# Optimization experiments

Measured on AMD Instinct MI355X. Metric: run time of the kernel, lower is better.

## Reference

```python
import jax, jax.numpy as jnp
import numpy as np

N, B, T, D, H = 200, 100, 256, 5, 20  # count_lstms, batch, seq_len, io units, lstm units


def setup_inputs() -> dict:
    key = jax.random.key(0)
    ks = jax.random.split(key, 4)
    inputs = jax.random.normal(ks[0], (B, T, D), dtype=jnp.float32)
    # Stacked per-LSTM parameters (Keras gate order: i, f, c, o)
    W = jax.random.normal(ks[1], (N, D, 4 * H), dtype=jnp.float32) * (1.0 / np.sqrt(D))
    U = jax.random.normal(ks[2], (N, H, 4 * H), dtype=jnp.float32) * (1.0 / np.sqrt(H))
    b = jnp.zeros((N, 4 * H), dtype=jnp.float32)
    dense_W = jax.random.normal(ks[3], (N * H, D), dtype=jnp.float32) * (1.0 / np.sqrt(N * H))
    dense_b = jnp.zeros((D,), dtype=jnp.float32)
    return {"inputs": inputs, "W": W, "U": U, "b": b, "dense_W": dense_W, "dense_b": dense_b}


def reference(inputs, W, U, b, dense_W, dense_b):
    # inputs: [B, T, D]; W: [N, D, 4H]; U: [N, H, 4H]; b: [N, 4H]
    n, h = W.shape[0], U.shape[1]
    batch = inputs.shape[0]
    x_t = jnp.transpose(inputs, (1, 0, 2))  # [T, B, D]
    h0 = jnp.zeros((n, batch, h), dtype=inputs.dtype)
    c0 = jnp.zeros((n, batch, h), dtype=inputs.dtype)

    def step(carry, xt):
        hprev, cprev = carry
        # gates for all N lstms at once: [N, B, 4H]
        z = (jnp.einsum('bd,ndk->nbk', xt, W)
             + jnp.einsum('nbh,nhk->nbk', hprev, U)
             + b[:, None, :])
        zi, zf, zg, zo = jnp.split(z, 4, axis=-1)
        i = jax.nn.sigmoid(zi)
        f = jax.nn.sigmoid(zf)
        g = jnp.tanh(zg)
        o = jax.nn.sigmoid(zo)
        cnew = f * cprev + i * g
        hnew = o * jnp.tanh(cnew)
        return (hnew, cnew), hnew

    (_, _), hs = jax.lax.scan(step, (h0, c0), x_t)  # hs: [T, N, B, H]
    # concat along feature axis -> [B, T, N*H]
    concat = jnp.transpose(hs, (2, 0, 1, 3)).reshape(batch, x_t.shape[0], n * h)
    out = concat @ dense_W + dense_b  # [B, T, D]
    return out
```

## Files before the change

kernel.cpp:

```cpp
#include <hip/hip_runtime.h>
#include <math.h>

constexpr int NL = 200;
constexpr int B  = 100;
constexpr int T  = 256;
constexpr int D  = 5;
constexpr int H  = 20;
constexpr int NW = 7;
constexpr int KP = 40;
constexpr int NWAVE = 5;
constexpr int BLKT  = 64 * NWAVE;
constexpr int BPAD  = 112;

constexpr int KX = 24;

typedef float  f32x4  __attribute__((ext_vector_type(4)));
typedef short  bf16x8 __attribute__((ext_vector_type(8)));

__device__ __forceinline__ float rcpf(float x) { return __builtin_amdgcn_rcpf(x); }

#if __has_builtin(__builtin_amdgcn_exp2f)
__device__ __forceinline__ float exp2fast(float x) { return __builtin_amdgcn_exp2f(x); }
#else
__device__ __forceinline__ float exp2fast(float x) { return __expf(x * 0.6931471805599453f); }
#endif

__device__ __forceinline__ unsigned short f2bf(float f) {
    union { float f; unsigned u; } v; v.f = f;
    unsigned r = v.u + 0x7fffu + ((v.u >> 16) & 1u);
    return (unsigned short)(r >> 16);
}
__device__ __forceinline__ unsigned pk2bf(float lo, float hi) {
    return (unsigned)f2bf(lo) | ((unsigned)f2bf(hi) << 16);
}

__device__ __forceinline__ void block_sync_lds() {
    asm volatile("s_waitcnt lgkmcnt(0)" ::: "memory");
    __builtin_amdgcn_s_barrier();
}

constexpr float NLOG2E = -1.4426950408889634f;
constexpr float TLOG2E = 2.8853900817779268f;

__global__ __launch_bounds__(256) void init_out_kernel(const float* __restrict__ dense_b,
                                                       float* __restrict__ out, int n) {
    int i = blockIdx.x * 256 + threadIdx.x;
    if (i < n) out[i] = dense_b[i % D];
}

__global__ __launch_bounds__(256) void xpack_kernel(const float* __restrict__ x,
                                                    int4* __restrict__ xe) {
    int i = blockIdx.x * 256 + threadIdx.x;
    if (i >= T * BPAD) return;
    const int t = i / BPAD;
    const int b = i % BPAD;
    int4 v = {0, 0, 0, 0};
    if (b < B) {
        const float* s = x + ((size_t)b * T + t) * D;
        v.x = (int)pk2bf(s[0], s[1]);
        v.y = (int)pk2bf(s[2], s[3]);
        v.z = (int)pk2bf(s[4], 0.0f);
        v.w = 0x00003F80;
    }
    xe[i] = v;
}

template<bool USE_WS>
__global__ __attribute__((amdgpu_flat_work_group_size(BLKT, BLKT)))
void lstm_mfma5_kernel(
    const int4*  __restrict__ xe,
    const float* __restrict__ Wg,
    const float* __restrict__ Ug,
    const float* __restrict__ bg,
    const float* __restrict__ dWg,
    float* __restrict__ pw,
    float* __restrict__ out)
{
    const int blk = blockIdx.x;
    const int n   = blk / NW;
    const int w   = blk % NW;
    const int tid = threadIdx.x;
    const int wid = tid >> 6;
    const int l   = tid & 63;
    const int c16 = l & 15;
    const int g4  = l >> 4;

    __shared__ __align__(16) short bcol[2][16][KP];

    for (int i = tid; i < 2 * 16 * KP / 2; i += BLKT)
        ((int*)&bcol[0][0][0])[i] = 0;

    const float* Un = Ug  + (size_t)n * H * 4 * H;
    const float* Wn = Wg  + (size_t)n * D * 4 * H;
    const float* bn = bg  + (size_t)n * 4 * H;
    const float* dn = dWg + (size_t)n * H * D;

    const int gateA = c16 & 3;
    const int hA4   = c16 >> 2;
    const float sA  = (gateA == 2) ? TLOG2E : NLOG2E;
    const int colA  = gateA * H + (wid * 4 + hA4);
    bf16x8 afrag;
    #pragma unroll
    for (int j = 0; j < 8; ++j) {
        const int k = 8 * g4 + j;
        float v = 0.0f;
        if (k < KX) {
            const int mt = k % 6, gg = k / 6;
            if (mt < 5) v = Un[(mt * 4 + gg) * 4 * H + colA];
        } else if (k < KX + D) {
            v = Wn[(k - KX) * 4 * H + colA];
        } else if (k == 30) {
            v = bn[colA];
        }
        afrag[j] = (short)f2bf(sA * v);
    }
    bf16x8 afrag_d = {};
    if (wid == 1) {
        #pragma unroll
        for (int j = 0; j < 8; ++j) {
            const int k = 8 * g4 + j;
            float v = 0.0f;
            if (c16 < D && k < KX) {
                const int mt = k % 6, gg = k / 6;
                if (mt < 5) v = dn[(mt * 4 + gg) * D + c16];
            }
            afrag_d[j] = (short)f2bf(v);
        }
    }

    const int  bgl    = w * 16 + c16;
    const bool bvalid = bgl < B;
    const int4* xq = xe + bgl;
    float* pwn = USE_WS ? (pw + (size_t)n * T * (D * B))
                        : (out + ((size_t)bgl * T) * D);

    __syncthreads();

    int4 xn4;
    if (wid == 0 && l < 16) {
        *(int4*)&bcol[0][c16][KX] = xq[0];
        xn4 = xq[(T > 1 ? 1 : 0) * BPAD];
    }
    __syncthreads();

    float cst = 0.0f;
    const f32x4 zero4 = {0.0f, 0.0f, 0.0f, 0.0f};
    int p = 0;

    for (int t = 0; t < T; ++t) {
        const bf16x8 bfrag = *(const bf16x8*)&bcol[p][c16][8 * g4];

        if (wid == 1) {
            const f32x4 accd = __builtin_amdgcn_mfma_f32_16x16x32_bf16(
                afrag_d, bfrag, zero4, 0, 0, 0);
            if (t > 0 && bvalid) {
                #pragma unroll
                for (int reg = 0; reg < 4; ++reg) {
                    const int d = g4 * 4 + reg;
                    if (d < D) {
                        if (USE_WS)
                            pwn[(size_t)(t - 1) * (D * B) + d * B + bgl] = accd[reg];
                        else
                            atomicAdd(&pwn[(size_t)(t - 1) * D + d], accd[reg]);
                    }
                }
            }
        }

        const f32x4 acc = __builtin_amdgcn_mfma_f32_16x16x32_bf16(
            afrag, bfrag, zero4, 0, 0, 0);
        const float iv = rcpf(1.0f + exp2fast(acc[0]));
        const float fv = rcpf(1.0f + exp2fast(acc[1]));
        const float gv = fmaf(-2.0f, rcpf(exp2fast(acc[2]) + 1.0f), 1.0f);
        const float ov = rcpf(1.0f + exp2fast(acc[3]));
        cst = fmaf(fv, cst, iv * gv);
        const float th = fmaf(-2.0f, rcpf(exp2fast(TLOG2E * cst) + 1.0f), 1.0f);
        const float hv = ov * th;

        bcol[p ^ 1][c16][g4 * 6 + wid] = (short)f2bf(hv);

        if (wid == 0 && l < 16) {
            *(int4*)&bcol[p ^ 1][c16][KX] = xn4;
            const int tc = (t + 2 < T) ? t + 2 : T - 1;
            xn4 = xq[(size_t)tc * BPAD];
        }

        block_sync_lds();
        p ^= 1;
    }

    if (wid == 1) {
        const bf16x8 bfrag = *(const bf16x8*)&bcol[p][c16][8 * g4];
        const f32x4 accd = __builtin_amdgcn_mfma_f32_16x16x32_bf16(
            afrag_d, bfrag, zero4, 0, 0, 0);
        if (bvalid) {
            #pragma unroll
            for (int reg = 0; reg < 4; ++reg) {
                const int d = g4 * 4 + reg;
                if (d < D) {
                    if (USE_WS)
                        pwn[(size_t)(T - 1) * (D * B) + d * B + bgl] = accd[reg];
                    else
                        atomicAdd(&pwn[(size_t)(T - 1) * D + d], accd[reg]);
                }
            }
        }
    }
}

__global__ __launch_bounds__(512) void reduce_kernel(
    const float* __restrict__ pw, const float* __restrict__ dense_b,
    float* __restrict__ out)
{
    const int t    = blockIdx.x;
    const int flat = threadIdx.x;
    if (flat >= B * D) return;
    const int d = flat / B;
    const int b = flat % B;
    const float* p = pw + (size_t)t * (D * B) + flat;
    constexpr size_t stride = (size_t)T * D * B;
    float a0 = 0.0f, a1 = 0.0f;
    #pragma unroll 10
    for (int n = 0; n < NL; n += 2) {
        a0 += p[(size_t)n * stride];
        a1 += p[(size_t)(n + 1) * stride];
    }
    out[((size_t)b * T + t) * D + d] = a0 + a1 + dense_b[d];
}

extern "C" void kernel_launch(void* const* d_in, const int* in_sizes, int n_in,
                              void* d_out, int out_size, void* d_ws, size_t ws_size,
                              hipStream_t stream) {
    const float* x   = (const float*)d_in[0];
    const float* Wg  = (const float*)d_in[1];
    const float* Ug  = (const float*)d_in[2];
    const float* bg  = (const float*)d_in[3];
    const float* dWg = (const float*)d_in[4];
    const float* dbv = (const float*)d_in[5];
    float* out = (float*)d_out;

    const size_t xe_bytes = (size_t)T * BPAD * sizeof(int4);
    const size_t pw_bytes = (size_t)NL * T * D * B * sizeof(float);

    int4* xe = (int4*)d_ws;
    xpack_kernel<<<(T * BPAD + 255) / 256, 256, 0, stream>>>(x, xe);

    if (ws_size >= xe_bytes + pw_bytes) {
        float* pw = (float*)((char*)d_ws + xe_bytes);
        lstm_mfma5_kernel<true><<<NL * NW, BLKT, 0, stream>>>(xe, Wg, Ug, bg, dWg, pw, out);
        reduce_kernel<<<T, 512, 0, stream>>>(pw, dbv, out);
    } else {
        init_out_kernel<<<(out_size + 255) / 256, 256, 0, stream>>>(dbv, out, out_size);
        lstm_mfma5_kernel<false><<<NL * NW, BLKT, 0, stream>>>(xe, Wg, Ug, bg, dWg, nullptr, out);
    }
}
```

Baseline: 219.9 us.

## Process two LSTMs per block to interleave independent recurrences

Each block now runs two independent LSTMs (n and n+100) side by side, with separate LDS buffers and state, and issues two MFMAs plus two activation chains per timestep under one barrier. The goal is to hide the latency of the serial MFMA→transcendental→LDS→barrier chain with independent work and to halve the number of barriers overall. The cost is more registers and LDS per block and half as many blocks (700 instead of 1400), which may reduce parallelism across the GPU.

```diff
diff --git a/kernel.cpp b/kernel.cpp
--- a/kernel.cpp
+++ b/kernel.cpp
@@ -11,6 +11,7 @@
 constexpr int NWAVE = 5;
 constexpr int BLKT  = 64 * NWAVE;
 constexpr int BPAD  = 112;
+constexpr int NPAIR = NL / 2;
 
 constexpr int KX = 24;
 
@@ -65,9 +66,19 @@
     xe[i] = v;
 }
 
+__device__ __forceinline__ float lstm_act(const f32x4 a, float& c) {
+    const float iv = rcpf(1.0f + exp2fast(a[0]));
+    const float fv = rcpf(1.0f + exp2fast(a[1]));
+    const float gv = fmaf(-2.0f, rcpf(exp2fast(a[2]) + 1.0f), 1.0f);
+    const float ov = rcpf(1.0f + exp2fast(a[3]));
+    c = fmaf(fv, c, iv * gv);
+    const float th = fmaf(-2.0f, rcpf(exp2fast(TLOG2E * c) + 1.0f), 1.0f);
+    return ov * th;
+}
+
 template<bool USE_WS>
 __global__ __attribute__((amdgpu_flat_work_group_size(BLKT, BLKT)))
-void lstm_mfma5_kernel(
+void lstm_mfma5x2_kernel(
     const int4*  __restrict__ xe,
     const float* __restrict__ Wg,
     const float* __restrict__ Ug,
@@ -77,45 +88,49 @@
     float* __restrict__ out)
 {
     const int blk = blockIdx.x;
-    const int n   = blk / NW;
+    const int pr  = blk / NW;
     const int w   = blk % NW;
+    const int n0  = pr;
+    const int n1  = pr + NPAIR;
     const int tid = threadIdx.x;
     const int wid = tid >> 6;
     const int l   = tid & 63;
     const int c16 = l & 15;
     const int g4  = l >> 4;
 
-    __shared__ __align__(16) short bcol[2][16][KP];
-
-    for (int i = tid; i < 2 * 16 * KP / 2; i += BLKT)
-        ((int*)&bcol[0][0][0])[i] = 0;
-
-    const float* Un = Ug  + (size_t)n * H * 4 * H;
-    const float* Wn = Wg  + (size_t)n * D * 4 * H;
-    const float* bn = bg  + (size_t)n * 4 * H;
-    const float* dn = dWg + (size_t)n * H * D;
+    __shared__ __align__(16) short bcol[2][2][16][KP];
+
+    for (int i = tid; i < 2 * 2 * 16 * KP / 2; i += BLKT)
+        ((int*)&bcol[0][0][0][0])[i] = 0;
 
     const int gateA = c16 & 3;
     const int hA4   = c16 >> 2;
     const float sA  = (gateA == 2) ? TLOG2E : NLOG2E;
-    const int colA  = gateA * H + (wid * 4 + hA4);
-    bf16x8 afrag;
-    #pragma unroll
-    for (int j = 0; j < 8; ++j) {
-        const int k = 8 * g4 + j;
-        float v = 0.0f;
-        if (k < KX) {
-            const int mt = k % 6, gg = k / 6;
-            if (mt < 5) v = Un[(mt * 4 + gg) * 4 * H + colA];
-        } else if (k < KX + D) {
-            v = Wn[(k - KX) * 4 * H + colA];
-        } else if (k == 30) {
-            v = bn[colA];
-        }
-        afrag[j] = (short)f2bf(sA * v);
-    }
-    bf16x8 afrag_d = {};
-    if (wid == 1) {
+    auto buildA = [&](int n) {
+        const float* Un = Ug + (size_t)n * H * 4 * H;
+        const float* Wn = Wg + (size_t)n * D * 4 * H;
+        const float* bn = bg + (size_t)n * 4 * H;
+        const int colA  = gateA * H + (wid * 4 + hA4);
+        bf16x8 a;
+        #pragma unroll
+        for (int j = 0; j < 8; ++j) {
+            const int k = 8 * g4 + j;
+            float v = 0.0f;
+            if (k < KX) {
+                const int mt = k % 6, gg = k / 6;
+                if (mt < 5) v = Un[(mt * 4 + gg) * 4 * H + colA];
+            } else if (k < KX + D) {
+                v = Wn[(k - KX) * 4 * H + colA];
+            } else if (k == 30) {
+                v = bn[colA];
+            }
+            a[j] = (short)f2bf(sA * v);
+        }
+        return a;
+    };
+    auto buildD = [&](int n) {
+        const float* dn = dWg + (size_t)n * H * D;
+        bf16x8 a;
         #pragma unroll
         for (int j = 0; j < 8; ++j) {
             const int k = 8 * g4 + j;
@@ -124,35 +139,46 @@
                 const int mt = k % 6, gg = k / 6;
                 if (mt < 5) v = dn[(mt * 4 + gg) * D + c16];
             }
-            afrag_d[j] = (short)f2bf(v);
-        }
-    }
+            a[j] = (short)f2bf(v);
+        }
+        return a;
+    };
+    const bf16x8 af0 = buildA(n0);
+    const bf16x8 af1 = buildA(n1);
+    bf16x8 afd = {};
+    if (wid == 1) afd = buildD(n0);
+    if (wid == 2) afd = buildD(n1);
 
     const int  bgl    = w * 16 + c16;
     const bool bvalid = bgl < B;
     const int4* xq = xe + bgl;
-    float* pwn = USE_WS ? (pw + (size_t)n * T * (D * B))
+    const int   dn_  = (wid == 2) ? n1 : n0;
+    float* pwn = USE_WS ? (pw + (size_t)dn_ * T * (D * B))
                         : (out + ((size_t)bgl * T) * D);
 
     __syncthreads();
 
     int4 xn4;
     if (wid == 0 && l < 16) {
-        *(int4*)&bcol[0][c16][KX] = xq[0];
+        const int4 x0 = xq[0];
+        *(int4*)&bcol[0][0][c16][KX] = x0;
+        *(int4*)&bcol[1][0][c16][KX] = x0;
         xn4 = xq[(T > 1 ? 1 : 0) * BPAD];
     }
     __syncthreads();
 
-    float cst = 0.0f;
+    float cst0 = 0.0f, cst1 = 0.0f;
     const f32x4 zero4 = {0.0f, 0.0f, 0.0f, 0.0f};
     int p = 0;
 
     for (int t = 0; t < T; ++t) {
-        const bf16x8 bfrag = *(const bf16x8*)&bcol[p][c16][8 * g4];
-
-        if (wid == 1) {
+        const bf16x8 bf0 = *(const bf16x8*)&bcol[0][p][c16][8 * g4];
+        const bf16x8 bf1 = *(const bf16x8*)&bcol[1][p][c16][8 * g4];
+
+        if (wid == 1 || wid == 2) {
+            const bf16x8 bfd = (wid == 1) ? bf0 : bf1;
             const f32x4 accd = __builtin_amdgcn_mfma_f32_16x16x32_bf16(
-                afrag_d, bfrag, zero4, 0, 0, 0);
+                afd, bfd, zero4, 0, 0, 0);
             if (t > 0 && bvalid) {
                 #pragma unroll
                 for (int reg = 0; reg < 4; ++reg) {
@@ -167,20 +193,17 @@
             }
         }
 
-        const f32x4 acc = __builtin_amdgcn_mfma_f32_16x16x32_bf16(
-            afrag, bfrag, zero4, 0, 0, 0);
-        const float iv = rcpf(1.0f + exp2fast(acc[0]));
-        const float fv = rcpf(1.0f + exp2fast(acc[1]));
-        const float gv = fmaf(-2.0f, rcpf(exp2fast(acc[2]) + 1.0f), 1.0f);
-        const float ov = rcpf(1.0f + exp2fast(acc[3]));
-        cst = fmaf(fv, cst, iv * gv);
-        const float th = fmaf(-2.0f, rcpf(exp2fast(TLOG2E * cst) + 1.0f), 1.0f);
-        const float hv = ov * th;
-
-        bcol[p ^ 1][c16][g4 * 6 + wid] = (short)f2bf(hv);
+        const f32x4 a0 = __builtin_amdgcn_mfma_f32_16x16x32_bf16(af0, bf0, zero4, 0, 0, 0);
+        const f32x4 a1 = __builtin_amdgcn_mfma_f32_16x16x32_bf16(af1, bf1, zero4, 0, 0, 0);
+        const float h0 = lstm_act(a0, cst0);
+        const float h1 = lstm_act(a1, cst1);
+
+        bcol[0][p ^ 1][c16][g4 * 6 + wid] = (short)f2bf(h0);
+        bcol[1][p ^ 1][c16][g4 * 6 + wid] = (short)f2bf(h1);
 
         if (wid == 0 && l < 16) {
-            *(int4*)&bcol[p ^ 1][c16][KX] = xn4;
+            *(int4*)&bcol[0][p ^ 1][c16][KX] = xn4;
+            *(int4*)&bcol[1][p ^ 1][c16][KX] = xn4;
             const int tc = (t + 2 < T) ? t + 2 : T - 1;
             xn4 = xq[(size_t)tc * BPAD];
         }
@@ -189,10 +212,10 @@
         p ^= 1;
     }
 
-    if (wid == 1) {
-        const bf16x8 bfrag = *(const bf16x8*)&bcol[p][c16][8 * g4];
+    if (wid == 1 || wid == 2) {
+        const bf16x8 bfd = *(const bf16x8*)&bcol[wid - 1][p][c16][8 * g4];
         const f32x4 accd = __builtin_amdgcn_mfma_f32_16x16x32_bf16(
-            afrag_d, bfrag, zero4, 0, 0, 0);
+            afd, bfd, zero4, 0, 0, 0);
         if (bvalid) {
             #pragma unroll
             for (int reg = 0; reg < 4; ++reg) {
@@ -247,10 +270,10 @@
 
     if (ws_size >= xe_bytes + pw_bytes) {
         float* pw = (float*)((char*)d_ws + xe_bytes);
-        lstm_mfma5_kernel<true><<<NL * NW, BLKT, 0, stream>>>(xe, Wg, Ug, bg, dWg, pw, out);
+        lstm_mfma5x2_kernel<true><<<NPAIR * NW, BLKT, 0, stream>>>(xe, Wg, Ug, bg, dWg, pw, out);
         reduce_kernel<<<T, 512, 0, stream>>>(pw, dbv, out);
     } else {
         init_out_kernel<<<(out_size + 255) / 256, 256, 0, stream>>>(dbv, out, out_size);
-        lstm_mfma5_kernel<false><<<NL * NW, BLKT, 0, stream>>>(xe, Wg, Ug, bg, dWg, nullptr, out);
-    }
-}
+        lstm_mfma5x2_kernel<false><<<NPAIR * NW, BLKT, 0, stream>>>(xe, Wg, Ug, bg, dWg, nullptr, out);
+    }
+}
```

Measured after the change: 215.5 us. 1.02x faster.
